# Kernel optimization log

Measured on AMD Instinct MI355X. Metric: run time of the kernel, lower is better.

## Reference

```python
import jax, jax.numpy as jnp
import numpy as np

DILATION = 64
KERNEL = 2

def setup_inputs() -> dict:
    key = jax.random.key(0)
    k1, k2 = jax.random.split(key)
    x = jax.random.normal(k1, (16, 64, 16384), dtype=jnp.float32)
    w = jax.random.normal(k2, (64, 64, KERNEL), dtype=jnp.float32) * 0.1
    return {"x": x, "w": w}

def _causal_dilated_conv(x, w):
    # left-pad by dilation*(kernel_size-1) for causality
    pad = DILATION * (KERNEL - 1)
    xp = jnp.pad(x, ((0, 0), (0, 0), (pad, 0)))
    return jax.lax.conv_general_dilated(
        xp, w,
        window_strides=(1,),
        padding='VALID',
        rhs_dilation=(DILATION,),
        dimension_numbers=('NCH', 'OIH', 'NCH'))

def reference(x, w):
    y = _causal_dilated_conv(x, w)          # [B, C_out, T]
    return jnp.tanh(y) * jax.nn.sigmoid(y)  # fused gate
```

## Files before the change

### kernel.cpp

```cpp
#include <hip/hip_runtime.h>


#define B_ 16
#define C_ 64
#define T_ 16384
#define TT 128
#define HALO 64
#define RR (TT + HALO)
#define S_ 66

typedef __attribute__((ext_vector_type(8))) short short8;
typedef __attribute__((ext_vector_type(4))) float f32x4;

union Frag { short8 s; unsigned u[4]; };

__device__ __forceinline__ unsigned bf16_rne(float f) {
    unsigned u = __float_as_uint(f);
    unsigned r = 0x7fffu + ((u >> 16) & 1u);
    return (u + r) >> 16;
}

__device__ __forceinline__ unsigned pack_hilo(float x) {
    unsigned hb = bf16_rne(x);
    float hf = __uint_as_float(hb << 16);
    unsigned lb = bf16_rne(x - hf);
    return hb | (lb << 16);
}

__global__ __launch_bounds__(256, 3) void conv_gate_mfma(
    const float* __restrict__ x,
    const float* __restrict__ w,
    float* __restrict__ out)
{
    __shared__ unsigned xs[RR * S_];

    const int tid = threadIdx.x;
    const int t0  = blockIdx.x * TT;
    const int b   = blockIdx.y;
    const float* xb = x + (size_t)b * C_ * T_;

    #pragma unroll
    for (int it = 0; it < 24; ++it) {
        int task = it * 256 + tid;
        int rr   = task % RR;
        int cp   = task / RR;
        int g    = t0 - HALO + rr;
        float a0 = 0.f, a1 = 0.f;
        if (g >= 0) {
            a0 = xb[(size_t)(2 * cp)     * T_ + g];
            a1 = xb[(size_t)(2 * cp + 1) * T_ + g];
        }
        unsigned p0 = pack_hilo(a0), p1 = pack_hilo(a1);
        *(uint2*)(&xs[rr * S_ + 2 * cp]) = make_uint2(p0, p1);
    }

    const int lane = tid & 63;
    const int wid  = tid >> 6;
    const int m    = lane & 15;
    const int q    = lane >> 4;
    const int co   = wid * 16 + m;

    Frag wh[2][2], wl[2][2];
    #pragma unroll
    for (int h = 0; h < 2; ++h) {
        const float* wp = w + co * 128 + h * 64 + q * 16;
        float f[16];
        #pragma unroll
        for (int v = 0; v < 4; ++v) {
            float4 t4 = *(const float4*)(wp + 4 * v);
            f[4*v+0] = t4.x; f[4*v+1] = t4.y; f[4*v+2] = t4.z; f[4*v+3] = t4.w;
        }
        #pragma unroll
        for (int p = 0; p < 2; ++p) {
            #pragma unroll
            for (int d = 0; d < 4; ++d) {
                float e0 = f[2*(2*d)   + p];
                float e1 = f[2*(2*d+1) + p];
                unsigned h0 = bf16_rne(e0), h1 = bf16_rne(e1);
                float r0 = e0 - __uint_as_float(h0 << 16);
                float r1 = e1 - __uint_as_float(h1 << 16);
                wh[p][h].u[d] = h0 | (h1 << 16);
                wl[p][h].u[d] = bf16_rne(r0) | (bf16_rne(r1) << 16);
            }
        }
    }

    f32x4 acc[8];
    #pragma unroll
    for (int s = 0; s < 8; ++s) acc[s] = (f32x4){0.f, 0.f, 0.f, 0.f};

    __syncthreads();

    const int n = m;
    #pragma unroll
    for (int s = 0; s < 8; ++s) {
        #pragma unroll
        for (int p = 0; p < 2; ++p) {
            int rr = 16 * s + n + 64 * p;
            const unsigned* rowp = &xs[rr * S_];
            #pragma unroll
            for (int h = 0; h < 2; ++h) {
                const unsigned* bp = rowp + 32 * h + 8 * q;
                uint2 d0 = *(const uint2*)(bp + 0);
                uint2 d1 = *(const uint2*)(bp + 2);
                uint2 d2 = *(const uint2*)(bp + 4);
                uint2 d3 = *(const uint2*)(bp + 6);
                Frag xh, xl;
                xh.u[0] = (d0.x & 0xffffu) | (d0.y << 16);
                xl.u[0] = (d0.x >> 16)     | (d0.y & 0xffff0000u);
                xh.u[1] = (d1.x & 0xffffu) | (d1.y << 16);
                xl.u[1] = (d1.x >> 16)     | (d1.y & 0xffff0000u);
                xh.u[2] = (d2.x & 0xffffu) | (d2.y << 16);
                xl.u[2] = (d2.x >> 16)     | (d2.y & 0xffff0000u);
                xh.u[3] = (d3.x & 0xffffu) | (d3.y << 16);
                xl.u[3] = (d3.x >> 16)     | (d3.y & 0xffff0000u);
                acc[s] = __builtin_amdgcn_mfma_f32_16x16x32_bf16(wh[p][h].s, xh.s, acc[s], 0, 0, 0);
                acc[s] = __builtin_amdgcn_mfma_f32_16x16x32_bf16(wh[p][h].s, xl.s, acc[s], 0, 0, 0);
                acc[s] = __builtin_amdgcn_mfma_f32_16x16x32_bf16(wl[p][h].s, xh.s, acc[s], 0, 0, 0);
            }
        }
    }

    float* ob = out + ((size_t)b * C_ + wid * 16) * T_ + t0;
    #pragma unroll
    for (int s = 0; s < 8; ++s) {
        #pragma unroll
        for (int r = 0; r < 4; ++r) {
            float y  = acc[s][r];
            float e  = __expf(-y);
            float e2 = e * e;
            float sig = __builtin_amdgcn_rcpf(1.f + e);
            float th  = 2.f * __builtin_amdgcn_rcpf(1.f + e2) - 1.f;
            ob[(size_t)(4 * q + r) * T_ + 16 * s + n] = th * sig;
        }
    }
}

extern "C" void kernel_launch(void* const* d_in, const int* in_sizes, int n_in,
                              void* d_out, int out_size, void* d_ws, size_t ws_size,
                              hipStream_t stream) {
    const float* x = (const float*)d_in[0];
    const float* w = (const float*)d_in[1];
    float* out = (float*)d_out;
    dim3 grid(T_ / TT, B_);
    conv_gate_mfma<<<grid, dim3(256), 0, stream>>>(x, w, out);
}
```

Before: 150.2 us.

## Split hi/lo bf16 planes in XOR-swizzled LDS and reuse fragments across taps

The shared tile now holds separate high and low bf16 planes with an XOR swizzle, so each B fragment is a single 16-byte LDS read instead of four reads followed by bit unpacking. The MFMA loop walks 12 row groups and reuses each loaded fragment for both dilation taps, which roughly halves LDS fragment loads. Staging uses truncation rather than RNE for the hi part and handles four channels per task. The gate epilogue is rewritten to need one reciprocal instead of two, with input clamping to keep it from overflowing.

Measured after the change: 131.5 us. 1.14x faster.

```diff
diff --git a/kernel.cpp b/kernel.cpp
--- a/kernel.cpp
+++ b/kernel.cpp
@@ -7,7 +7,7 @@
 #define TT 128
 #define HALO 64
 #define RR (TT + HALO)
-#define S_ 66
+#define XL_OFS (RR * 64)
 
 typedef __attribute__((ext_vector_type(8))) short short8;
 typedef __attribute__((ext_vector_type(4))) float f32x4;
@@ -20,19 +20,12 @@
     return (u + r) >> 16;
 }
 
-__device__ __forceinline__ unsigned pack_hilo(float x) {
-    unsigned hb = bf16_rne(x);
-    float hf = __uint_as_float(hb << 16);
-    unsigned lb = bf16_rne(x - hf);
-    return hb | (lb << 16);
-}
-
-__global__ __launch_bounds__(256, 3) void conv_gate_mfma(
+__global__ __launch_bounds__(256, 3) void conv_gate_mfma2(
     const float* __restrict__ x,
     const float* __restrict__ w,
     float* __restrict__ out)
 {
-    __shared__ unsigned xs[RR * S_];
+    __shared__ unsigned short xs[2 * RR * 64];
 
     const int tid = threadIdx.x;
     const int t0  = blockIdx.x * TT;
@@ -40,18 +33,30 @@
     const float* xb = x + (size_t)b * C_ * T_;
 
     #pragma unroll
-    for (int it = 0; it < 24; ++it) {
+    for (int it = 0; it < 12; ++it) {
         int task = it * 256 + tid;
         int rr   = task % RR;
-        int cp   = task / RR;
+        int c4   = task / RR;
         int g    = t0 - HALO + rr;
-        float a0 = 0.f, a1 = 0.f;
+        float v0 = 0.f, v1 = 0.f, v2 = 0.f, v3 = 0.f;
         if (g >= 0) {
-            a0 = xb[(size_t)(2 * cp)     * T_ + g];
-            a1 = xb[(size_t)(2 * cp + 1) * T_ + g];
+            const float* xp = xb + (size_t)(4 * c4) * T_ + g;
+            v0 = xp[0 * T_]; v1 = xp[1 * T_]; v2 = xp[2 * T_]; v3 = xp[3 * T_];
         }
-        unsigned p0 = pack_hilo(a0), p1 = pack_hilo(a1);
-        *(uint2*)(&xs[rr * S_ + 2 * cp]) = make_uint2(p0, p1);
+        unsigned u0 = __float_as_uint(v0), u1 = __float_as_uint(v1);
+        unsigned u2 = __float_as_uint(v2), u3 = __float_as_uint(v3);
+        unsigned h01 = (u0 >> 16) | (u1 & 0xffff0000u);
+        unsigned h23 = (u2 >> 16) | (u3 & 0xffff0000u);
+        unsigned l0 = __float_as_uint(v0 - __uint_as_float(u0 & 0xffff0000u));
+        unsigned l1 = __float_as_uint(v1 - __uint_as_float(u1 & 0xffff0000u));
+        unsigned l2 = __float_as_uint(v2 - __uint_as_float(u2 & 0xffff0000u));
+        unsigned l3 = __float_as_uint(v3 - __uint_as_float(u3 & 0xffff0000u));
+        unsigned g01 = (l0 >> 16) | (l1 & 0xffff0000u);
+        unsigned g23 = (l2 >> 16) | (l3 & 0xffff0000u);
+        int chunk = (c4 >> 1) ^ (rr & 7);
+        int so = rr * 64 + chunk * 8 + (c4 & 1) * 4;
+        *(uint2*)(&xs[so])          = make_uint2(h01, h23);
+        *(uint2*)(&xs[XL_OFS + so]) = make_uint2(g01, g23);
     }
 
     const int lane = tid & 63;
@@ -91,32 +96,33 @@
 
     __syncthreads();
 
-    const int n = m;
+    const int n  = m;
+    const int sw = n & 7;
     #pragma unroll
-    for (int s = 0; s < 8; ++s) {
+    for (int u = 0; u < 12; ++u) {
+        const int rbase = (16 * u + n) * 64;
+        Frag fh[2], fl[2];
         #pragma unroll
-        for (int p = 0; p < 2; ++p) {
-            int rr = 16 * s + n + 64 * p;
-            const unsigned* rowp = &xs[rr * S_];
+        for (int h = 0; h < 2; ++h) {
+            int c = (((4 * h + q) ^ sw) * 8);
+            fh[h].s = *(const short8*)(&xs[rbase + c]);
+            fl[h].s = *(const short8*)(&xs[XL_OFS + rbase + c]);
+        }
+        if (u < 8) {
             #pragma unroll
             for (int h = 0; h < 2; ++h) {
-                const unsigned* bp = rowp + 32 * h + 8 * q;
-                uint2 d0 = *(const uint2*)(bp + 0);
-                uint2 d1 = *(const uint2*)(bp + 2);
-                uint2 d2 = *(const uint2*)(bp + 4);
-                uint2 d3 = *(const uint2*)(bp + 6);
-                Frag xh, xl;
-                xh.u[0] = (d0.x & 0xffffu) | (d0.y << 16);
-                xl.u[0] = (d0.x >> 16)     | (d0.y & 0xffff0000u);
-                xh.u[1] = (d1.x & 0xffffu) | (d1.y << 16);
-                xl.u[1] = (d1.x >> 16)     | (d1.y & 0xffff0000u);
-                xh.u[2] = (d2.x & 0xffffu) | (d2.y << 16);
-                xl.u[2] = (d2.x >> 16)     | (d2.y & 0xffff0000u);
-                xh.u[3] = (d3.x & 0xffffu) | (d3.y << 16);
-                xl.u[3] = (d3.x >> 16)     | (d3.y & 0xffff0000u);
-                acc[s] = __builtin_amdgcn_mfma_f32_16x16x32_bf16(wh[p][h].s, xh.s, acc[s], 0, 0, 0);
-                acc[s] = __builtin_amdgcn_mfma_f32_16x16x32_bf16(wh[p][h].s, xl.s, acc[s], 0, 0, 0);
-                acc[s] = __builtin_amdgcn_mfma_f32_16x16x32_bf16(wl[p][h].s, xh.s, acc[s], 0, 0, 0);
+                acc[u] = __builtin_amdgcn_mfma_f32_16x16x32_bf16(wh[0][h].s, fh[h].s, acc[u], 0, 0, 0);
+                acc[u] = __builtin_amdgcn_mfma_f32_16x16x32_bf16(wh[0][h].s, fl[h].s, acc[u], 0, 0, 0);
+                acc[u] = __builtin_amdgcn_mfma_f32_16x16x32_bf16(wl[0][h].s, fh[h].s, acc[u], 0, 0, 0);
+            }
+        }
+        if (u >= 4) {
+            const int s2 = u - 4;
+            #pragma unroll
+            for (int h = 0; h < 2; ++h) {
+                acc[s2] = __builtin_amdgcn_mfma_f32_16x16x32_bf16(wh[1][h].s, fh[h].s, acc[s2], 0, 0, 0);
+                acc[s2] = __builtin_amdgcn_mfma_f32_16x16x32_bf16(wh[1][h].s, fl[h].s, acc[s2], 0, 0, 0);
+                acc[s2] = __builtin_amdgcn_mfma_f32_16x16x32_bf16(wl[1][h].s, fh[h].s, acc[s2], 0, 0, 0);
             }
         }
     }
@@ -127,11 +133,12 @@
         #pragma unroll
         for (int r = 0; r < 4; ++r) {
             float y  = acc[s][r];
-            float e  = __expf(-y);
-            float e2 = e * e;
-            float sig = __builtin_amdgcn_rcpf(1.f + e);
-            float th  = 2.f * __builtin_amdgcn_rcpf(1.f + e2) - 1.f;
-            ob[(size_t)(4 * q + r) * T_ + 16 * s + n] = th * sig;
+            y = fminf(fmaxf(y, -20.f), 20.f);
+            float e   = __expf(-y);
+            float e2  = e * e;
+            float num = 1.f - e2;
+            float den = (1.f + e) * (1.f + e2);
+            ob[(size_t)(4 * q + r) * T_ + 16 * s + n] = num * __builtin_amdgcn_rcpf(den);
         }
     }
 }
@@ -143,5 +150,5 @@
     const float* w = (const float*)d_in[1];
     float* out = (float*)d_out;
     dim3 grid(T_ / TT, B_);
-    conv_gate_mfma<<<grid, dim3(256), 0, stream>>>(x, w, out);
+    conv_gate_mfma2<<<grid, dim3(256), 0, stream>>>(x, w, out);
 }
```
